# Performance work log

Measured on AMD Instinct MI355X. Metric: run time of the kernel, lower is better.

## Reference

```python
import jax, jax.numpy as jnp
import numpy as np

B, S, H = 1, 2048, 2560
NH, NKV, HD, FF = 20, 5, 128, 6912
EPS = 1e-5
ROPE_THETA = 500000.0


def rms_norm(x, w):
    return x * jax.lax.rsqrt(jnp.mean(x * x, axis=-1, keepdims=True) + EPS) * w


def bitlinear(x, w):
    # per-token int8 activation fake-quant
    s = jnp.clip(jnp.max(jnp.abs(x), axis=-1, keepdims=True), 1e-5, None)
    xq = jnp.clip(jnp.round(x * (127.0 / s)), -128.0, 127.0) * (s / 127.0)
    # per-tensor ternary weight fake-quant
    ws = jnp.clip(jnp.mean(jnp.abs(w)), 1e-5, None)
    wq = jnp.clip(jnp.round(w / ws), -1.0, 1.0) * ws
    return xq @ wq.T


def rotate_half(x):
    x1, x2 = jnp.split(x, 2, axis=-1)
    return jnp.concatenate([-x2, x1], axis=-1)


def setup_inputs() -> dict:
    key = jax.random.key(0)
    ks = jax.random.split(key, 8)
    std = 0.02
    hidden_states = jax.random.normal(ks[0], (B, S, H), jnp.float32)
    # real RoPE tables (the torch harness fed rand; we use the model's rope)
    pos = jnp.arange(S, dtype=jnp.float32)
    inv_freq = 1.0 / (ROPE_THETA ** (jnp.arange(0, HD, 2, dtype=jnp.float32) / HD))
    freqs = pos[:, None] * inv_freq[None, :]
    emb = jnp.concatenate([freqs, freqs], axis=-1)  # [S, HD]
    cos = jnp.cos(emb)[None]
    sin = jnp.sin(emb)[None]
    return {
        "hidden_states": hidden_states,
        "cos": cos,
        "sin": sin,
        "w_in_ln": jnp.ones((H,), jnp.float32),
        "w_q": jax.random.normal(ks[1], (NH * HD, H), jnp.float32) * std,
        "w_k": jax.random.normal(ks[2], (NKV * HD, H), jnp.float32) * std,
        "w_v": jax.random.normal(ks[3], (NKV * HD, H), jnp.float32) * std,
        "w_o": jax.random.normal(ks[4], (H, NH * HD), jnp.float32) * std,
        "w_attn_sub": jnp.ones((H,), jnp.float32),
        "w_post_ln": jnp.ones((H,), jnp.float32),
        "w_gate": jax.random.normal(ks[5], (FF, H), jnp.float32) * std,
        "w_up": jax.random.normal(ks[6], (FF, H), jnp.float32) * std,
        "w_ffn_sub": jnp.ones((FF,), jnp.float32),
        "w_down": jax.random.normal(ks[7], (H, FF), jnp.float32) * std,
    }


def reference(hidden_states, cos, sin, w_in_ln, w_q, w_k, w_v, w_o,
              w_attn_sub, w_post_ln, w_gate, w_up, w_ffn_sub, w_down):
    # --- self-attention block ---
    residual = hidden_states
    x = rms_norm(hidden_states, w_in_ln)
    q = bitlinear(x, w_q).reshape(B, S, NH, HD).transpose(0, 2, 1, 3)   # [B,NH,S,HD]
    k = bitlinear(x, w_k).reshape(B, S, NKV, HD).transpose(0, 2, 1, 3)  # [B,NKV,S,HD]
    v = bitlinear(x, w_v).reshape(B, S, NKV, HD).transpose(0, 2, 1, 3)
    c = cos[:, None]  # [B,1,S,HD]
    s = sin[:, None]
    q = q * c + rotate_half(q) * s
    k = k * c + rotate_half(k) * s
    k = jnp.repeat(k, NH // NKV, axis=1)  # GQA expand -> [B,NH,S,HD]
    v = jnp.repeat(v, NH // NKV, axis=1)
    scores = jnp.einsum('bhqd,bhkd->bhqk', q, k) / np.sqrt(HD).astype(np.float32)
    causal = jnp.tril(jnp.ones((S, S), bool))
    scores = jnp.where(causal, scores, jnp.float32(-1e30))
    attn = jax.nn.softmax(scores, axis=-1)
    o = jnp.einsum('bhqk,bhkd->bhqd', attn, v).transpose(0, 2, 1, 3).reshape(B, S, H)
    o = bitlinear(rms_norm(o, w_attn_sub), w_o)  # sub-norm before o_proj
    h = residual + o
    # --- MLP block (relu^2 gated) ---
    residual = h
    x = rms_norm(h, w_post_ln)
    g = bitlinear(x, w_gate)
    u = bitlinear(x, w_up)
    m = jnp.square(jax.nn.relu(g)) * u
    m = bitlinear(rms_norm(m, w_ffn_sub), w_down)  # sub-norm before down_proj
    return residual + m
```

## Files before the change

kernel.cpp:

```cpp
#include <hip/hip_runtime.h>

#define S_ 2048
#define H_ 2560
#define NH_ 20
#define NKV_ 5
#define HD_ 128
#define FF_ 6912
#define EPS_ 1e-5f

typedef __bf16 bf16;
typedef _Float16 f16;
typedef __bf16 bf16x8 __attribute__((ext_vector_type(8)));
typedef _Float16 f16x8 __attribute__((ext_vector_type(8)));
typedef float f32x4 __attribute__((ext_vector_type(4)));

__device__ inline float waveSum(float v) {
#pragma unroll
    for (int off = 32; off > 0; off >>= 1) v += __shfl_down(v, off);
    return v;
}
__device__ inline float waveMax(float v) {
#pragma unroll
    for (int off = 32; off > 0; off >>= 1) v = fmaxf(v, __shfl_down(v, off));
    return v;
}

__global__ void k_absmean(const float* __restrict__ w, int n, float* __restrict__ out) {
    __shared__ float red[4];
    float p = 0.f;
    for (int i = blockIdx.x * blockDim.x + threadIdx.x; i < n; i += gridDim.x * blockDim.x)
        p += fabsf(w[i]);
    p = waveSum(p);
    if ((threadIdx.x & 63) == 0) red[threadIdx.x >> 6] = p;
    __syncthreads();
    if (threadIdx.x == 0) atomicAdd(out, red[0] + red[1] + red[2] + red[3]);
}

__global__ void k_quant_w(const float* __restrict__ w, int n,
                          const float* __restrict__ sum, float inv_n,
                          bf16* __restrict__ wq) {
    float ws = fmaxf(sum[0] * inv_n, 1e-5f);
    for (int i = blockIdx.x * blockDim.x + threadIdx.x; i < n; i += gridDim.x * blockDim.x) {
        float q = rintf(w[i] / ws);
        q = fminf(fmaxf(q, -1.f), 1.f);
        wq[i] = (bf16)q;
    }
}

__global__ void k_rms_quant(const float* __restrict__ x, const float* __restrict__ wln,
                            int n, bf16* __restrict__ xq, float* __restrict__ a_scale) {
    extern __shared__ float sx[];
    float* red = sx + n;
    int row = blockIdx.x, tid = threadIdx.x;
    const float* xr = x + (size_t)row * n;
    float p = 0.f;
    for (int i = tid; i < n; i += 256) { float v = xr[i]; sx[i] = v; p += v * v; }
    p = waveSum(p);
    if ((tid & 63) == 0) red[tid >> 6] = p;
    __syncthreads();
    float ssum = red[0] + red[1] + red[2] + red[3];
    float rms = rsqrtf(ssum * (1.0f / n) + EPS_);
    __syncthreads();
    float mx = 0.f;
    for (int i = tid; i < n; i += 256) {
        float xv = sx[i] * rms * wln[i];
        sx[i] = xv;
        mx = fmaxf(mx, fabsf(xv));
    }
    mx = waveMax(mx);
    if ((tid & 63) == 0) red[tid >> 6] = mx;
    __syncthreads();
    float s = fmaxf(fmaxf(fmaxf(red[0], red[1]), fmaxf(red[2], red[3])), 1e-5f);
    if (tid == 0) a_scale[row] = s * (1.0f / 127.0f);
    float qs = 127.0f / s;
    for (int i = tid; i < n; i += 256) {
        float q = rintf(sx[i] * qs);
        q = fminf(fmaxf(q, -128.f), 127.f);
        xq[(size_t)row * n + i] = (bf16)q;
    }
}

__global__ __launch_bounds__(256) void k_gemm_bt(
    const bf16* __restrict__ A, const bf16* __restrict__ Bw,
    int M, int N, int K,
    const float* __restrict__ a_scale, const float* __restrict__ ws_sum, float inv_n,
    const float* __restrict__ add, const float* __restrict__ gprev,
    float* __restrict__ outF) {
    __shared__ bf16 As[128 * 72];
    __shared__ bf16 Bs[128 * 72];
    int tid = threadIdx.x;
    int lane = tid & 63, w = tid >> 6;
    int quad = lane >> 4, l15 = lane & 15;
    int wm = w >> 1, wn = w & 1;
    int m0 = blockIdx.y * 128, n0 = blockIdx.x * 128;
    f32x4 acc[4][4] = {};
    int ar = tid >> 3, ac = (tid & 7) * 8;
    const bf16* Ag = A + (size_t)m0 * K;
    const bf16* Bg = Bw + (size_t)n0 * K;
    for (int kt = 0; kt < K; kt += 64) {
        __syncthreads();
#pragma unroll
        for (int ppp = 0; ppp < 4; ppp++) {
            int r = ar + ppp * 32;
            *(bf16x8*)&As[r * 72 + ac] = *(const bf16x8*)(Ag + (size_t)r * K + kt + ac);
            *(bf16x8*)&Bs[r * 72 + ac] = *(const bf16x8*)(Bg + (size_t)r * K + kt + ac);
        }
        __syncthreads();
#pragma unroll
        for (int kc = 0; kc < 2; kc++) {
            bf16x8 af[4], bfr[4];
#pragma unroll
            for (int i = 0; i < 4; i++)
                af[i] = *(const bf16x8*)&As[(wm * 64 + i * 16 + l15) * 72 + kc * 32 + quad * 8];
#pragma unroll
            for (int j = 0; j < 4; j++)
                bfr[j] = *(const bf16x8*)&Bs[(wn * 64 + j * 16 + l15) * 72 + kc * 32 + quad * 8];
#pragma unroll
            for (int i = 0; i < 4; i++)
#pragma unroll
                for (int j = 0; j < 4; j++)
                    acc[i][j] = __builtin_amdgcn_mfma_f32_16x16x32_bf16(af[i], bfr[j], acc[i][j], 0, 0, 0);
        }
    }
    float ws = fmaxf(ws_sum[0] * inv_n, 1e-5f);
#pragma unroll
    for (int i = 0; i < 4; i++) {
        int rowb = m0 + wm * 64 + i * 16 + quad * 4;
#pragma unroll
        for (int j = 0; j < 4; j++) {
            int col = n0 + wn * 64 + j * 16 + l15;
#pragma unroll
            for (int r = 0; r < 4; r++) {
                int row = rowb + r;
                float val = a_scale[row] * ws * acc[i][j][r];
                size_t off = (size_t)row * N + col;
                if (add) val += add[off];
                if (gprev) {
                    float gv = fmaxf(gprev[off], 0.f);
                    val = gv * gv * val;
                }
                outF[off] = val;
            }
        }
    }
}

__global__ void k_rope_split(const float* __restrict__ xin, f16* __restrict__ xh,
                             f16* __restrict__ xl, const float* __restrict__ cosp,
                             const float* __restrict__ sinp, int nh) {
    int idx = blockIdx.x * 256 + threadIdx.x;
    int d = idx & 63;
    int t = idx >> 6;
    int h = t % nh;
    int s = t / nh;
    size_t base = (size_t)s * (nh * HD_) + h * HD_;
    float x1 = xin[base + d], x2 = xin[base + d + 64];
    float c1 = cosp[s * HD_ + d], s1 = sinp[s * HD_ + d];
    float c2 = cosp[s * HD_ + d + 64], s2 = sinp[s * HD_ + d + 64];
    float y1 = x1 * c1 - x2 * s1;
    float y2 = x2 * c2 + x1 * s2;
    f16 h1 = (f16)y1, h2 = (f16)y2;
    xh[base + d] = h1;
    xl[base + d] = (f16)(y1 - (float)h1);
    xh[base + d + 64] = h2;
    xl[base + d + 64] = (f16)(y2 - (float)h2);
}

__global__ void k_split(const float* __restrict__ x, f16* __restrict__ xh,
                        f16* __restrict__ xl, int n) {
    int i = blockIdx.x * 256 + threadIdx.x;
    if (i < n) {
        float v = x[i];
        f16 h = (f16)v;
        xh[i] = h;
        xl[i] = (f16)(v - (float)h);
    }
}

__global__ __launch_bounds__(256) void k_attn(
    const f16* __restrict__ qhp, const f16* __restrict__ qlp,
    const f16* __restrict__ khp, const f16* __restrict__ klp,
    const f16* __restrict__ vhp, const f16* __restrict__ vlp,
    float* __restrict__ o) {
    __shared__ f16 Kth[32][136], Ktl[32][136];
    __shared__ f16 Vth[128][40], Vtl[128][40];
    __shared__ f16 Pth[4][16][40], Ptl[4][16][40];
    int tid = threadIdx.x;
    int w = tid >> 6, lane = tid & 63, quad = lane >> 4, l15 = lane & 15;
    int head = blockIdx.y;
    int q0 = blockIdx.x * 64;
    int kvh = head >> 2;

    f16x8 qfh[4], qfl[4];
    {
        int qrow = q0 + w * 16 + l15;
        const f16* qp = qhp + (size_t)qrow * (NH_ * HD_) + head * HD_ + quad * 8;
        const f16* qp2 = qlp + (size_t)qrow * (NH_ * HD_) + head * HD_ + quad * 8;
#pragma unroll
        for (int kc = 0; kc < 4; kc++) {
            qfh[kc] = *(const f16x8*)(qp + kc * 32);
            qfl[kc] = *(const f16x8*)(qp2 + kc * 32);
        }
    }
    f32x4 oacc[8] = {};
    float m_i[4], l_i[4];
#pragma unroll
    for (int r = 0; r < 4; r++) { m_i[r] = -3.0e38f; l_i[r] = 0.f; }
    int sr = tid >> 3, scb = (tid & 7) * 16;
    int nkt = (q0 + 64) >> 5;
    for (int kt = 0; kt < nkt; kt++) {
        int key0 = kt * 32;
        __syncthreads();
        {
            size_t koff = (size_t)(key0 + sr) * (NKV_ * HD_) + kvh * HD_ + scb;
            *(f16x8*)&Kth[sr][scb] = *(const f16x8*)(khp + koff);
            *(f16x8*)&Kth[sr][scb + 8] = *(const f16x8*)(khp + koff + 8);
            *(f16x8*)&Ktl[sr][scb] = *(const f16x8*)(klp + koff);
            *(f16x8*)&Ktl[sr][scb + 8] = *(const f16x8*)(klp + koff + 8);
            f16x8 v0 = *(const f16x8*)(vhp + koff), v1 = *(const f16x8*)(vhp + koff + 8);
            f16x8 w0 = *(const f16x8*)(vlp + koff), w1 = *(const f16x8*)(vlp + koff + 8);
#pragma unroll
            for (int j = 0; j < 8; j++) {
                Vth[scb + j][sr] = v0[j];
                Vth[scb + 8 + j][sr] = v1[j];
                Vtl[scb + j][sr] = w0[j];
                Vtl[scb + 8 + j][sr] = w1[j];
            }
        }
        __syncthreads();
        f32x4 sc[2] = {};
#pragma unroll
        for (int kn = 0; kn < 2; kn++)
#pragma unroll
            for (int kc = 0; kc < 4; kc++) {
                f16x8 kfh = *(const f16x8*)&Kth[kn * 16 + l15][kc * 32 + quad * 8];
                f16x8 kfl = *(const f16x8*)&Ktl[kn * 16 + l15][kc * 32 + quad * 8];
                sc[kn] = __builtin_amdgcn_mfma_f32_16x16x32_f16(qfh[kc], kfh, sc[kn], 0, 0, 0);
                sc[kn] = __builtin_amdgcn_mfma_f32_16x16x32_f16(qfh[kc], kfl, sc[kn], 0, 0, 0);
                sc[kn] = __builtin_amdgcn_mfma_f32_16x16x32_f16(qfl[kc], kfh, sc[kn], 0, 0, 0);
            }
        const float scale = 0.08838834764831845f;
#pragma unroll
        for (int r = 0; r < 4; r++) {
            int qr = q0 + w * 16 + quad * 4 + r;
            float s0 = sc[0][r] * scale, s1 = sc[1][r] * scale;
            if (key0 + l15 > qr) s0 = -1e30f;
            if (key0 + 16 + l15 > qr) s1 = -1e30f;
            float mx = fmaxf(s0, s1);
#pragma unroll
            for (int off = 8; off > 0; off >>= 1) mx = fmaxf(mx, __shfl_xor(mx, off));
            float mnew = fmaxf(m_i[r], mx);
            float alpha = expf(m_i[r] - mnew);
            m_i[r] = mnew;
            l_i[r] *= alpha;
#pragma unroll
            for (int dn = 0; dn < 8; dn++) oacc[dn][r] *= alpha;
            float p0 = expf(s0 - mnew), p1 = expf(s1 - mnew);
            l_i[r] += p0 + p1;
            f16 ph0 = (f16)p0, ph1 = (f16)p1;
            Pth[w][quad * 4 + r][l15] = ph0;
            Pth[w][quad * 4 + r][16 + l15] = ph1;
            Ptl[w][quad * 4 + r][l15] = (f16)(p0 - (float)ph0);
            Ptl[w][quad * 4 + r][16 + l15] = (f16)(p1 - (float)ph1);
        }
        __syncthreads();
        f16x8 pfh = *(const f16x8*)&Pth[w][l15][quad * 8];
        f16x8 pfl = *(const f16x8*)&Ptl[w][l15][quad * 8];
#pragma unroll
        for (int dn = 0; dn < 8; dn++) {
            f16x8 vfh = *(const f16x8*)&Vth[dn * 16 + l15][quad * 8];
            f16x8 vfl = *(const f16x8*)&Vtl[dn * 16 + l15][quad * 8];
            oacc[dn] = __builtin_amdgcn_mfma_f32_16x16x32_f16(pfh, vfh, oacc[dn], 0, 0, 0);
            oacc[dn] = __builtin_amdgcn_mfma_f32_16x16x32_f16(pfh, vfl, oacc[dn], 0, 0, 0);
            oacc[dn] = __builtin_amdgcn_mfma_f32_16x16x32_f16(pfl, vfh, oacc[dn], 0, 0, 0);
        }
    }
    float linv[4];
#pragma unroll
    for (int r = 0; r < 4; r++) {
        float lt = l_i[r];
#pragma unroll
        for (int off = 8; off > 0; off >>= 1) lt += __shfl_xor(lt, off);
        linv[r] = 1.0f / lt;
    }
#pragma unroll
    for (int dn = 0; dn < 8; dn++)
#pragma unroll
        for (int r = 0; r < 4; r++) {
            int row = q0 + w * 16 + quad * 4 + r;
            o[(size_t)row * (NH_ * HD_) + head * HD_ + dn * 16 + l15] = oacc[dn][r] * linv[r];
        }
}

extern "C" void kernel_launch(void* const* d_in, const int* in_sizes, int n_in,
                              void* d_out, int out_size, void* d_ws, size_t ws_size,
                              hipStream_t stream) {
    const float* hidden   = (const float*)d_in[0];
    const float* cosp     = (const float*)d_in[1];
    const float* sinp     = (const float*)d_in[2];
    const float* w_in_ln  = (const float*)d_in[3];
    const float* w_q      = (const float*)d_in[4];
    const float* w_k      = (const float*)d_in[5];
    const float* w_v      = (const float*)d_in[6];
    const float* w_o      = (const float*)d_in[7];
    const float* w_attn   = (const float*)d_in[8];
    const float* w_post   = (const float*)d_in[9];
    const float* w_gate   = (const float*)d_in[10];
    const float* w_up     = (const float*)d_in[11];
    const float* w_ffn    = (const float*)d_in[12];
    const float* w_down   = (const float*)d_in[13];
    float* out = (float*)d_out;

    const size_t SH = (size_t)S_ * H_;
    const size_t SKV = (size_t)S_ * NKV_ * HD_;

    char* p = (char*)d_ws;
    auto alloc = [&](size_t b) { char* r = p; p += (b + 255) & ~(size_t)255; return r; };
    float* sums   = (float*)alloc(64 * 4);
    float* ascale = (float*)alloc(S_ * 4);
    bf16* wqb     = (bf16*)alloc((size_t)FF_ * H_ * 2);
    bf16* xq      = (bf16*)alloc(SH * 2);
    bf16* xqf     = (bf16*)alloc((size_t)S_ * FF_ * 2);
    float* hbuf   = (float*)alloc(SH * 4);
    char* reg     = alloc(62914560);
    float* q   = (float*)reg;
    float* kf  = (float*)(reg + 20971520);
    float* vf  = (float*)(reg + 26214400);
    f16* qhb   = (f16*)(reg + 31457280);
    f16* qlb   = (f16*)(reg + 41943040);
    f16* khb   = (f16*)(reg + 52428800);
    f16* klb   = (f16*)(reg + 55050240);
    f16* vhb   = (f16*)(reg + 57671680);
    f16* vlb   = (f16*)(reg + 60293120);
    float* ob  = (float*)reg;
    float* mbuf = (float*)reg;

    hipMemsetAsync(sums, 0, 64 * 4, stream);
    const int nQ = NH_ * HD_ * H_, nKV = NKV_ * HD_ * H_, nG = FF_ * H_;
    k_absmean<<<512, 256, 0, stream>>>(w_q, nQ, sums + 0);
    k_absmean<<<512, 256, 0, stream>>>(w_k, nKV, sums + 1);
    k_absmean<<<512, 256, 0, stream>>>(w_v, nKV, sums + 2);
    k_absmean<<<512, 256, 0, stream>>>(w_o, nQ, sums + 3);
    k_absmean<<<512, 256, 0, stream>>>(w_gate, nG, sums + 4);
    k_absmean<<<512, 256, 0, stream>>>(w_up, nG, sums + 5);
    k_absmean<<<512, 256, 0, stream>>>(w_down, nG, sums + 6);

    k_rms_quant<<<S_, 256, (H_ + 64) * 4, stream>>>(hidden, w_in_ln, H_, xq, ascale);

    k_quant_w<<<2048, 256, 0, stream>>>(w_q, nQ, sums + 0, 1.0f / nQ, wqb);
    k_gemm_bt<<<dim3(NH_ * HD_ / 128, S_ / 128), 256, 0, stream>>>(
        xq, wqb, S_, NH_ * HD_, H_, ascale, sums + 0, 1.0f / nQ, nullptr, nullptr, q);
    k_quant_w<<<2048, 256, 0, stream>>>(w_k, nKV, sums + 1, 1.0f / nKV, wqb);
    k_gemm_bt<<<dim3(NKV_ * HD_ / 128, S_ / 128), 256, 0, stream>>>(
        xq, wqb, S_, NKV_ * HD_, H_, ascale, sums + 1, 1.0f / nKV, nullptr, nullptr, kf);
    k_quant_w<<<2048, 256, 0, stream>>>(w_v, nKV, sums + 2, 1.0f / nKV, wqb);
    k_gemm_bt<<<dim3(NKV_ * HD_ / 128, S_ / 128), 256, 0, stream>>>(
        xq, wqb, S_, NKV_ * HD_, H_, ascale, sums + 2, 1.0f / nKV, nullptr, nullptr, vf);

    k_rope_split<<<S_ * NH_ * 64 / 256, 256, 0, stream>>>(q, qhb, qlb, cosp, sinp, NH_);
    k_rope_split<<<S_ * NKV_ * 64 / 256, 256, 0, stream>>>(kf, khb, klb, cosp, sinp, NKV_);
    k_split<<<(int)(SKV / 256), 256, 0, stream>>>(vf, vhb, vlb, (int)SKV);

    k_attn<<<dim3(S_ / 64, NH_), 256, 0, stream>>>(qhb, qlb, khb, klb, vhb, vlb, ob);

    k_rms_quant<<<S_, 256, (H_ + 64) * 4, stream>>>(ob, w_attn, H_, xq, ascale);
    k_quant_w<<<2048, 256, 0, stream>>>(w_o, nQ, sums + 3, 1.0f / nQ, wqb);
    k_gemm_bt<<<dim3(H_ / 128, S_ / 128), 256, 0, stream>>>(
        xq, wqb, S_, H_, NH_ * HD_, ascale, sums + 3, 1.0f / nQ, hidden, nullptr, hbuf);

    k_rms_quant<<<S_, 256, (H_ + 64) * 4, stream>>>(hbuf, w_post, H_, xq, ascale);
    k_quant_w<<<4096, 256, 0, stream>>>(w_gate, nG, sums + 4, 1.0f / nG, wqb);
    k_gemm_bt<<<dim3(FF_ / 128, S_ / 128), 256, 0, stream>>>(
        xq, wqb, S_, FF_, H_, ascale, sums + 4, 1.0f / nG, nullptr, nullptr, mbuf);
    k_quant_w<<<4096, 256, 0, stream>>>(w_up, nG, sums + 5, 1.0f / nG, wqb);
    k_gemm_bt<<<dim3(FF_ / 128, S_ / 128), 256, 0, stream>>>(
        xq, wqb, S_, FF_, H_, ascale, sums + 5, 1.0f / nG, nullptr, mbuf, mbuf);

    k_rms_quant<<<S_, 256, (FF_ + 64) * 4, stream>>>(mbuf, w_ffn, FF_, xqf, ascale);

    k_quant_w<<<4096, 256, 0, stream>>>(w_down, nG, sums + 6, 1.0f / nG, wqb);
    k_gemm_bt<<<dim3(H_ / 128, S_ / 128), 256, 0, stream>>>(
        xqf, wqb, S_, H_, FF_, ascale, sums + 6, 1.0f / nG, hbuf, nullptr, out);
}
```

Baseline: 1.783 ms.

## Load K/V fragments straight from global memory, pre-transpose V, reverse query tile order

Attention no longer stages K and V tiles in shared memory behind block-wide barriers. Each wave now loads its MFMA K fragments directly from global memory, and V is pre-transposed into a [kv*dim, seq] f16 hi/lo layout by a new k_vtrans kernel so the PV fragments become contiguous global loads. Query tiles are launched in reverse order so the longest causal blocks start first, which should balance the tail. The cost is redundant global/L2 traffic, since each of the four waves reloads the same K/V, plus an extra transpose kernel with strided reads. Removing the barrier before P is re-read is safe because each wave reads only its own P slice.

After: 2.157 ms. 21.0% more time.

```diff
diff --git a/kernel.cpp b/kernel.cpp
--- a/kernel.cpp
+++ b/kernel.cpp
@@ -166,78 +166,64 @@
     xl[base + d + 64] = (f16)(y2 - (float)h2);
 }
 
-__global__ void k_split(const float* __restrict__ x, f16* __restrict__ xh,
-                        f16* __restrict__ xl, int n) {
-    int i = blockIdx.x * 256 + threadIdx.x;
-    if (i < n) {
-        float v = x[i];
-        f16 h = (f16)v;
-        xh[i] = h;
-        xl[i] = (f16)(v - (float)h);
-    }
+__global__ void k_vtrans(const float* __restrict__ vf, f16* __restrict__ vth,
+                         f16* __restrict__ vtl) {
+    int col = blockIdx.x;
+    int s = blockIdx.y * 256 + threadIdx.x;
+    float v = vf[(size_t)s * (NKV_ * HD_) + col];
+    f16 h = (f16)v;
+    vth[(size_t)col * S_ + s] = h;
+    vtl[(size_t)col * S_ + s] = (f16)(v - (float)h);
 }
 
 __global__ __launch_bounds__(256) void k_attn(
     const f16* __restrict__ qhp, const f16* __restrict__ qlp,
     const f16* __restrict__ khp, const f16* __restrict__ klp,
-    const f16* __restrict__ vhp, const f16* __restrict__ vlp,
+    const f16* __restrict__ vth, const f16* __restrict__ vtl,
     float* __restrict__ o) {
-    __shared__ f16 Kth[32][136], Ktl[32][136];
-    __shared__ f16 Vth[128][40], Vtl[128][40];
     __shared__ f16 Pth[4][16][40], Ptl[4][16][40];
     int tid = threadIdx.x;
     int w = tid >> 6, lane = tid & 63, quad = lane >> 4, l15 = lane & 15;
     int head = blockIdx.y;
-    int q0 = blockIdx.x * 64;
+    int qt = gridDim.x - 1 - blockIdx.x;
+    int q0 = qt * 64;
     int kvh = head >> 2;
+    const int KVSTR = NKV_ * HD_;
 
     f16x8 qfh[4], qfl[4];
     {
         int qrow = q0 + w * 16 + l15;
-        const f16* qp = qhp + (size_t)qrow * (NH_ * HD_) + head * HD_ + quad * 8;
-        const f16* qp2 = qlp + (size_t)qrow * (NH_ * HD_) + head * HD_ + quad * 8;
+        size_t qoff = (size_t)qrow * (NH_ * HD_) + head * HD_ + quad * 8;
 #pragma unroll
         for (int kc = 0; kc < 4; kc++) {
-            qfh[kc] = *(const f16x8*)(qp + kc * 32);
-            qfl[kc] = *(const f16x8*)(qp2 + kc * 32);
+            qfh[kc] = *(const f16x8*)(qhp + qoff + kc * 32);
+            qfl[kc] = *(const f16x8*)(qlp + qoff + kc * 32);
         }
     }
     f32x4 oacc[8] = {};
     float m_i[4], l_i[4];
 #pragma unroll
     for (int r = 0; r < 4; r++) { m_i[r] = -3.0e38f; l_i[r] = 0.f; }
-    int sr = tid >> 3, scb = (tid & 7) * 16;
     int nkt = (q0 + 64) >> 5;
     for (int kt = 0; kt < nkt; kt++) {
         int key0 = kt * 32;
-        __syncthreads();
-        {
-            size_t koff = (size_t)(key0 + sr) * (NKV_ * HD_) + kvh * HD_ + scb;
-            *(f16x8*)&Kth[sr][scb] = *(const f16x8*)(khp + koff);
-            *(f16x8*)&Kth[sr][scb + 8] = *(const f16x8*)(khp + koff + 8);
-            *(f16x8*)&Ktl[sr][scb] = *(const f16x8*)(klp + koff);
-            *(f16x8*)&Ktl[sr][scb + 8] = *(const f16x8*)(klp + koff + 8);
-            f16x8 v0 = *(const f16x8*)(vhp + koff), v1 = *(const f16x8*)(vhp + koff + 8);
-            f16x8 w0 = *(const f16x8*)(vlp + koff), w1 = *(const f16x8*)(vlp + koff + 8);
-#pragma unroll
-            for (int j = 0; j < 8; j++) {
-                Vth[scb + j][sr] = v0[j];
-                Vth[scb + 8 + j][sr] = v1[j];
-                Vtl[scb + j][sr] = w0[j];
-                Vtl[scb + 8 + j][sr] = w1[j];
+        f16x8 kfh[2][4], kfl[2][4];
+#pragma unroll
+        for (int kn = 0; kn < 2; kn++)
+#pragma unroll
+            for (int kc = 0; kc < 4; kc++) {
+                size_t ka = (size_t)(key0 + kn * 16 + l15) * KVSTR + kvh * HD_ + kc * 32 + quad * 8;
+                kfh[kn][kc] = *(const f16x8*)(khp + ka);
+                kfl[kn][kc] = *(const f16x8*)(klp + ka);
             }
-        }
-        __syncthreads();
         f32x4 sc[2] = {};
 #pragma unroll
         for (int kn = 0; kn < 2; kn++)
 #pragma unroll
             for (int kc = 0; kc < 4; kc++) {
-                f16x8 kfh = *(const f16x8*)&Kth[kn * 16 + l15][kc * 32 + quad * 8];
-                f16x8 kfl = *(const f16x8*)&Ktl[kn * 16 + l15][kc * 32 + quad * 8];
-                sc[kn] = __builtin_amdgcn_mfma_f32_16x16x32_f16(qfh[kc], kfh, sc[kn], 0, 0, 0);
-                sc[kn] = __builtin_amdgcn_mfma_f32_16x16x32_f16(qfh[kc], kfl, sc[kn], 0, 0, 0);
-                sc[kn] = __builtin_amdgcn_mfma_f32_16x16x32_f16(qfl[kc], kfh, sc[kn], 0, 0, 0);
+                sc[kn] = __builtin_amdgcn_mfma_f32_16x16x32_f16(qfh[kc], kfh[kn][kc], sc[kn], 0, 0, 0);
+                sc[kn] = __builtin_amdgcn_mfma_f32_16x16x32_f16(qfh[kc], kfl[kn][kc], sc[kn], 0, 0, 0);
+                sc[kn] = __builtin_amdgcn_mfma_f32_16x16x32_f16(qfl[kc], kfh[kn][kc], sc[kn], 0, 0, 0);
             }
         const float scale = 0.08838834764831845f;
 #pragma unroll
@@ -263,13 +249,13 @@
             Ptl[w][quad * 4 + r][l15] = (f16)(p0 - (float)ph0);
             Ptl[w][quad * 4 + r][16 + l15] = (f16)(p1 - (float)ph1);
         }
-        __syncthreads();
         f16x8 pfh = *(const f16x8*)&Pth[w][l15][quad * 8];
         f16x8 pfl = *(const f16x8*)&Ptl[w][l15][quad * 8];
 #pragma unroll
         for (int dn = 0; dn < 8; dn++) {
-            f16x8 vfh = *(const f16x8*)&Vth[dn * 16 + l15][quad * 8];
-            f16x8 vfl = *(const f16x8*)&Vtl[dn * 16 + l15][quad * 8];
+            size_t va = (size_t)kvh * HD_ * S_ + (size_t)(dn * 16 + l15) * S_ + key0 + quad * 8;
+            f16x8 vfh = *(const f16x8*)(vth + va);
+            f16x8 vfl = *(const f16x8*)(vtl + va);
             oacc[dn] = __builtin_amdgcn_mfma_f32_16x16x32_f16(pfh, vfh, oacc[dn], 0, 0, 0);
             oacc[dn] = __builtin_amdgcn_mfma_f32_16x16x32_f16(pfh, vfl, oacc[dn], 0, 0, 0);
             oacc[dn] = __builtin_amdgcn_mfma_f32_16x16x32_f16(pfl, vfh, oacc[dn], 0, 0, 0);
@@ -330,8 +316,8 @@
     f16* qlb   = (f16*)(reg + 41943040);
     f16* khb   = (f16*)(reg + 52428800);
     f16* klb   = (f16*)(reg + 55050240);
-    f16* vhb   = (f16*)(reg + 57671680);
-    f16* vlb   = (f16*)(reg + 60293120);
+    f16* vthb  = (f16*)(reg + 57671680);
+    f16* vtlb  = (f16*)(reg + 60293120);
     float* ob  = (float*)reg;
     float* mbuf = (float*)reg;
 
@@ -359,9 +345,9 @@
 
     k_rope_split<<<S_ * NH_ * 64 / 256, 256, 0, stream>>>(q, qhb, qlb, cosp, sinp, NH_);
     k_rope_split<<<S_ * NKV_ * 64 / 256, 256, 0, stream>>>(kf, khb, klb, cosp, sinp, NKV_);
-    k_split<<<(int)(SKV / 256), 256, 0, stream>>>(vf, vhb, vlb, (int)SKV);
-
-    k_attn<<<dim3(S_ / 64, NH_), 256, 0, stream>>>(qhb, qlb, khb, klb, vhb, vlb, ob);
+    k_vtrans<<<dim3(NKV_ * HD_, S_ / 256), 256, 0, stream>>>(vf, vthb, vtlb);
+
+    k_attn<<<dim3(S_ / 64, NH_), 256, 0, stream>>>(qhb, qlb, khb, klb, vthb, vtlb, ob);
 
     k_rms_quant<<<S_, 256, (H_ + 64) * 4, stream>>>(ob, w_attn, H_, xq, ascale);
     k_quant_w<<<2048, 256, 0, stream>>>(w_o, nQ, sums + 3, 1.0f / nQ, wqb);
```
